# Kernel optimization log

Measured on AMD Instinct MI355X. Metric: run time of the kernel, lower is better.

## Reference

```python
import jax, jax.numpy as jnp
import numpy as np

BLOCK = 32       # MX block size
EMAX_E4M3 = 8.0  # max exponent of fp8 e4m3 (max normal = 448 = 1.75 * 2^8)
NUM_HEADS = 16


def _e4m3_round(v):
    """Round values to fp8 e4m3 grid (bias 7, 3 mantissa bits, subnormals, max 448)."""
    absv = jnp.abs(v)
    e = jnp.floor(jnp.log2(jnp.where(absv > 0, absv, 1.0)))
    e = jnp.maximum(e, -6.0)                # min normal exponent; below -> subnormal grid
    step = jnp.exp2(e - 3.0)                # 3 mantissa bits
    q = jnp.round(v / step) * step          # round-half-even like IEEE
    q = jnp.clip(q, -448.0, 448.0)
    return jnp.where(absv > 0, q, jnp.zeros_like(q))


def _mx_quantize(x):
    """Blockwise (32 along last dim) shared-exponent (E8M0) fp8 e4m3 quant-dequant."""
    shp = x.shape
    xb = x.reshape(shp[:-1] + (shp[-1] // BLOCK, BLOCK))
    amax = jnp.max(jnp.abs(xb), axis=-1, keepdims=True)
    sexp = jnp.floor(jnp.log2(jnp.where(amax > 0, amax, 1.0))) - EMAX_E4M3
    sexp = jnp.clip(sexp, -127.0, 127.0)    # E8M0 scale range
    scale = jnp.where(amax > 0, jnp.exp2(sexp), jnp.ones_like(sexp))
    q = _e4m3_round(xb / scale) * scale
    return q.reshape(shp)


def mxq(x):
    return _mx_quantize(x)


def _mx_linear(x, W, b):
    # quantize activations and weights (blocks of 32 along the contraction dim)
    return jnp.einsum('bse,oe->bso', mxq(x), mxq(W)) + b


def setup_inputs() -> dict:
    key = jax.random.key(0)
    ks = jax.random.split(key, 9)
    B, S, E = 4, 1024, 1024
    inp = {
        'query': jax.random.normal(ks[0], (B, S, E), dtype=jnp.float32),
        'Wq': jax.random.normal(ks[1], (E, E), dtype=jnp.float32) * 0.02,
        'bq': jnp.zeros((E,), dtype=jnp.float32),
        'Wk': jax.random.normal(ks[2], (E, E), dtype=jnp.float32) * 0.02,
        'bk': jnp.zeros((E,), dtype=jnp.float32),
        'Wv': jax.random.normal(ks[3], (E, E), dtype=jnp.float32) * 0.02,
        'bv': jnp.zeros((E,), dtype=jnp.float32),
        'Wo': jax.random.normal(ks[4], (E, E), dtype=jnp.float32) * 0.02,
        'bo': jnp.zeros((E,), dtype=jnp.float32),
    }
    return inp


def reference(query, Wq, bq, Wk, bk, Wv, bv, Wo, bo):
    B, S, E = query.shape
    H = NUM_HEADS
    D = E // H
    Q = _mx_linear(query, Wq, bq).reshape(B, S, H, D).transpose(0, 2, 1, 3)
    K = _mx_linear(query, Wk, bk).reshape(B, S, H, D).transpose(0, 2, 1, 3)
    V = _mx_linear(query, Wv, bv).reshape(B, S, H, D).transpose(0, 2, 1, 3)
    scores = jnp.einsum('bhqd,bhkd->bhqk', Q, K) / jnp.sqrt(jnp.float32(D))
    scores = mxq(scores)                    # score quantizer (blocks of 32 along kv dim)
    attn = jax.nn.softmax(scores, axis=-1)  # dropout p=0 -> identity
    ctx = jnp.einsum('bhqk,bhkd->bhqd', attn, V)
    ctx = ctx.transpose(0, 2, 1, 3).reshape(B, S, E)
    return _mx_linear(ctx, Wo, bo)
```

## Files before the change

kernel.cpp:

```cpp
#include <hip/hip_runtime.h>
#include <hip/hip_bf16.h>
#include <cstdint>
#include <cstddef>


#define S_LEN 1024
#define E_DIM 1024
#define NH    16
#define DH    64
#define BATCH 4
#define NROWS (BATCH * S_LEN)

typedef short          bf16x8  __attribute__((ext_vector_type(8)));
typedef float          f32x4   __attribute__((ext_vector_type(4)));
typedef unsigned short u16x8   __attribute__((ext_vector_type(8)));
typedef unsigned short u16x4   __attribute__((ext_vector_type(4)));
typedef unsigned int   u32x4   __attribute__((ext_vector_type(4)));


__device__ __forceinline__ void mx_scale_bits(float amax, float& scale, float& inv) {
  int eb = (int)(__float_as_uint(amax) >> 23);
  int sb = eb - 8;
  sb = sb < 1 ? 1 : (sb > 253 ? 253 : sb);
  float sc = __uint_as_float((unsigned)sb << 23);
  float iv = __uint_as_float((unsigned)(254 - sb) << 23);
  bool nz = (amax > 0.0f);
  scale = nz ? sc : 1.0f;
  inv   = nz ? iv : 1.0f;
}

__device__ __forceinline__ void qdq2(float& a, float& b) {
  a = fminf(fmaxf(a, -448.0f), 448.0f);
  b = fminf(fmaxf(b, -448.0f), 448.0f);
  int p = __builtin_amdgcn_cvt_pk_fp8_f32(a, b, 0, false);
  a = __builtin_amdgcn_cvt_f32_fp8(p, 0);
  b = __builtin_amdgcn_cvt_f32_fp8(p, 1);
}

__device__ __forceinline__ unsigned short f32_to_bf16_rne(float f) {
  unsigned u = __float_as_uint(f);
  unsigned r = 0x7FFFu + ((u >> 16) & 1u);
  return (unsigned short)((u + r) >> 16);
}

__device__ __forceinline__ float quad_red_max(float x) {
  auto p = __builtin_amdgcn_permlane16_swap(__float_as_uint(x), __float_as_uint(x), false, false);
  x = fmaxf(__uint_as_float(p[0]), __uint_as_float(p[1]));
  auto q = __builtin_amdgcn_permlane32_swap(__float_as_uint(x), __float_as_uint(x), false, false);
  return fmaxf(__uint_as_float(q[0]), __uint_as_float(q[1]));
}
__device__ __forceinline__ float quad_red_min(float x) {
  auto p = __builtin_amdgcn_permlane16_swap(__float_as_uint(x), __float_as_uint(x), false, false);
  x = fminf(__uint_as_float(p[0]), __uint_as_float(p[1]));
  auto q = __builtin_amdgcn_permlane32_swap(__float_as_uint(x), __float_as_uint(x), false, false);
  return fminf(__uint_as_float(q[0]), __uint_as_float(q[1]));
}
__device__ __forceinline__ float quad_red_sum(float x) {
  auto p = __builtin_amdgcn_permlane16_swap(__float_as_uint(x), __float_as_uint(x), false, false);
  x = __uint_as_float(p[0]) + __uint_as_float(p[1]);
  auto q = __builtin_amdgcn_permlane32_swap(__float_as_uint(x), __float_as_uint(x), false, false);
  return __uint_as_float(q[0]) + __uint_as_float(q[1]);
}


__device__ __forceinline__ void mxq_body(const float* __restrict__ in,
                                         unsigned short* __restrict__ out, int b) {
  const float4* p = (const float4*)(in + (size_t)b * 32);
  float v[32];
#pragma unroll
  for (int g = 0; g < 8; ++g) {
    float4 t = p[g];
    v[g * 4 + 0] = t.x; v[g * 4 + 1] = t.y; v[g * 4 + 2] = t.z; v[g * 4 + 3] = t.w;
  }
  float amax = 0.0f;
#pragma unroll
  for (int i = 0; i < 32; ++i) amax = fmaxf(amax, __builtin_fabsf(v[i]));
  float scale, inv;
  mx_scale_bits(amax, scale, inv);
  u16x8* q = (u16x8*)(out + (size_t)b * 32);
#pragma unroll
  for (int g = 0; g < 4; ++g) {
    u16x8 o;
#pragma unroll
    for (int e = 0; e < 8; e += 2) {
      float a = v[g * 8 + e] * inv, c = v[g * 8 + e + 1] * inv;
      qdq2(a, c);
      o[e]     = (unsigned short)(__float_as_uint(a * scale) >> 16);
      o[e + 1] = (unsigned short)(__float_as_uint(c * scale) >> 16);
    }
    q[g] = o;
  }
}

__global__ __launch_bounds__(256)
void mxq_all(const float* __restrict__ x,
             const float* __restrict__ w0, const float* __restrict__ w1,
             const float* __restrict__ w2, const float* __restrict__ w3,
             unsigned short* __restrict__ ox,
             unsigned short* __restrict__ o0, unsigned short* __restrict__ o1,
             unsigned short* __restrict__ o2, unsigned short* __restrict__ o3) {
  int blk = blockIdx.x;
  const float* in;
  unsigned short* out;
  int base;
  if (blk < 512)      { in = x;  out = ox; base = blk; }
  else if (blk < 640) { in = w0; out = o0; base = blk - 512; }
  else if (blk < 768) { in = w1; out = o1; base = blk - 640; }
  else if (blk < 896) { in = w2; out = o2; base = blk - 768; }
  else                { in = w3; out = o3; base = blk - 896; }
  mxq_body(in, out, base * 256 + threadIdx.x);
}


__global__ __launch_bounds__(256)
void gemm_qkv(const unsigned short* __restrict__ XQ,
              const unsigned short* __restrict__ Wqw, const unsigned short* __restrict__ Wkw,
              const unsigned short* __restrict__ Wvw,
              const float* __restrict__ bq, const float* __restrict__ bk,
              const float* __restrict__ bv,
              unsigned short* __restrict__ Qhi, unsigned short* __restrict__ Qlo,
              unsigned short* __restrict__ Khi, unsigned short* __restrict__ Klo,
              unsigned short* __restrict__ Vthi, unsigned short* __restrict__ Vtlo) {
  const int z = blockIdx.z;
  const unsigned short* Bw = (z == 0) ? Wqw : (z == 1) ? Wkw : Wvw;
  const float* bias = (z == 0) ? bq : (z == 1) ? bk : bv;
  unsigned short* Phi = (z == 0) ? Qhi : (z == 1) ? Khi : Vthi;
  unsigned short* Plo = (z == 0) ? Qlo : (z == 1) ? Klo : Vtlo;
  const float pre = (z == 0) ? 0.125f : 1.0f;

  __shared__ unsigned short sA[2][128 * 64];
  __shared__ unsigned short sB[2][128 * 64];
  const int tid = threadIdx.x;
  const int w = tid >> 6, ln = tid & 63;
  const int fid = blockIdx.y * 8 + blockIdx.x;
  const int xcd = fid & 7, sq = fid >> 3;
  const int bm = (xcd * 4 + (sq & 3)) * 128, bn = (sq >> 2) * 128;
  const int wm = (w >> 1) * 64, wn = (w & 1) * 64;
  const int quad = ln >> 4, col = ln & 15;

  f32x4 acc[4][4];
  f32x4 zero = {0.0f, 0.0f, 0.0f, 0.0f};
#pragma unroll
  for (int i = 0; i < 4; ++i)
#pragma unroll
    for (int j = 0; j < 4; ++j) acc[i][j] = zero;

  const int srow = ln >> 3;
  const int gsw  = (ln & 7) ^ srow;
  const int xo0 = (quad ^ (ln & 7)) * 8;
  const int xo1 = ((quad ^ 4) ^ (ln & 7)) * 8;

  auto STAGE = [&](int bb, int k0) {
#pragma unroll
    for (int q = 0; q < 4; ++q) {
      int row = w * 32 + q * 8 + srow;
      const unsigned short* ga = XQ + (size_t)(bm + row) * 1024 + k0 + gsw * 8;
      const unsigned short* gb = Bw + (size_t)(bn + row) * 1024 + k0 + gsw * 8;
      __builtin_amdgcn_global_load_lds(
          (const __attribute__((address_space(1))) unsigned int*)ga,
          (__attribute__((address_space(3))) unsigned int*)(&sA[bb][0] + (w * 32 + q * 8) * 64),
          16, 0, 0);
      __builtin_amdgcn_global_load_lds(
          (const __attribute__((address_space(1))) unsigned int*)gb,
          (__attribute__((address_space(3))) unsigned int*)(&sB[bb][0] + (w * 32 + q * 8) * 64),
          16, 0, 0);
    }
  };

  STAGE(0, 0);
#pragma unroll 1
  for (int k0 = 0; k0 < 1024; k0 += 64) {
    const int cur = (k0 >> 6) & 1;
    if (k0 < 960) {
      STAGE(cur ^ 1, k0 + 64);
      asm volatile("s_waitcnt vmcnt(8)" ::: "memory");
    } else {
      asm volatile("s_waitcnt vmcnt(0)" ::: "memory");
    }
    __builtin_amdgcn_s_barrier();
    __builtin_amdgcn_sched_barrier(0);

    const unsigned short* pA = &sA[cur][0];
    const unsigned short* pB = &sB[cur][0];
#pragma unroll
    for (int ks = 0; ks < 2; ++ks) {
      const int xo = ks ? xo1 : xo0;
      bf16x8 af[4], bfr[4];
#pragma unroll
      for (int t = 0; t < 4; ++t) {
        af[t]  = *(const bf16x8*)(pA + (wm + t * 16 + col) * 64 + xo);
        bfr[t] = *(const bf16x8*)(pB + (wn + t * 16 + col) * 64 + xo);
      }
#pragma unroll
      for (int ti = 0; ti < 4; ++ti)
#pragma unroll
        for (int tj = 0; tj < 4; ++tj)
          acc[ti][tj] = __builtin_amdgcn_mfma_f32_16x16x32_bf16(af[ti], bfr[tj], acc[ti][tj], 0, 0, 0);
    }
    __builtin_amdgcn_sched_barrier(0);
    __builtin_amdgcn_s_barrier();
  }

#pragma unroll
  for (int ti = 0; ti < 4; ++ti) {
#pragma unroll
    for (int tj = 0; tj < 4; ++tj) {
      int n = bn + wn + tj * 16 + col;
      float bv_ = bias[n];
      if (z != 2) {
#pragma unroll
        for (int i = 0; i < 4; ++i) {
          int m = bm + wm + ti * 16 + quad * 4 + i;
          float v = (acc[ti][tj][i] + bv_) * pre;
          unsigned short h = f32_to_bf16_rne(v);
          float hf = __uint_as_float((unsigned)h << 16);
          Phi[(size_t)m * 1024 + n] = h;
          Plo[(size_t)m * 1024 + n] = f32_to_bf16_rne(v - hf);
        }
      } else {
        int m0 = bm + wm + ti * 16 + quad * 4;
        u16x4 h4, l4;
#pragma unroll
        for (int i = 0; i < 4; ++i) {
          float v = acc[ti][tj][i] + bv_;
          unsigned short h = f32_to_bf16_rne(v);
          float hf = __uint_as_float((unsigned)h << 16);
          h4[i] = h;
          l4[i] = f32_to_bf16_rne(v - hf);
        }
        size_t idx = ((size_t)((m0 >> 10) * 1024 + n)) * 1024 + (m0 & 1023);
        *(u16x4*)(Phi + idx) = h4;
        *(u16x4*)(Plo + idx) = l4;
      }
    }
  }
}


__global__ __launch_bounds__(256)
void gemm_o(const unsigned short* __restrict__ A, const unsigned short* __restrict__ Bw,
            const float* __restrict__ bias, float* __restrict__ C) {
  __shared__ unsigned short sA[2][64 * 64];
  __shared__ unsigned short sB[2][128 * 64];
  const int tid = threadIdx.x;
  const int w = tid >> 6, ln = tid & 63;
  const int fid = blockIdx.y * 8 + blockIdx.x;
  const int xcd = fid & 7, sq = fid >> 3;
  const int bm = (xcd * 8 + (sq & 7)) * 64, bn = (sq >> 3) * 128;
  const int wr = (w >> 1) * 32, wc = (w & 1) * 64;
  const int quad = ln >> 4, col = ln & 15;

  f32x4 acc[2][4];
  f32x4 zero = {0.0f, 0.0f, 0.0f, 0.0f};
#pragma unroll
  for (int i = 0; i < 2; ++i)
#pragma unroll
    for (int j = 0; j < 4; ++j) acc[i][j] = zero;

  const int srow = ln >> 3;
  const int gsw  = (ln & 7) ^ srow;
  const int xo0 = (quad ^ (ln & 7)) * 8;
  const int xo1 = ((quad ^ 4) ^ (ln & 7)) * 8;

  auto STAGE = [&](int bb, int k0) {
#pragma unroll
    for (int qa = 0; qa < 2; ++qa) {
      int row = w * 16 + qa * 8 + srow;
      __builtin_amdgcn_global_load_lds(
          (const __attribute__((address_space(1))) unsigned int*)(A + (size_t)(bm + row) * 1024 + k0 + gsw * 8),
          (__attribute__((address_space(3))) unsigned int*)(&sA[bb][0] + (w * 16 + qa * 8) * 64),
          16, 0, 0);
    }
#pragma unroll
    for (int qb = 0; qb < 4; ++qb) {
      int row = w * 32 + qb * 8 + srow;
      __builtin_amdgcn_global_load_lds(
          (const __attribute__((address_space(1))) unsigned int*)(Bw + (size_t)(bn + row) * 1024 + k0 + gsw * 8),
          (__attribute__((address_space(3))) unsigned int*)(&sB[bb][0] + (w * 32 + qb * 8) * 64),
          16, 0, 0);
    }
  };

  STAGE(0, 0);
#pragma unroll 1
  for (int k0 = 0; k0 < 1024; k0 += 64) {
    const int cur = (k0 >> 6) & 1;
    if (k0 < 960) {
      STAGE(cur ^ 1, k0 + 64);
      asm volatile("s_waitcnt vmcnt(6)" ::: "memory");
    } else {
      asm volatile("s_waitcnt vmcnt(0)" ::: "memory");
    }
    __builtin_amdgcn_s_barrier();
    __builtin_amdgcn_sched_barrier(0);

    const unsigned short* pA = &sA[cur][0];
    const unsigned short* pB = &sB[cur][0];
#pragma unroll
    for (int ks = 0; ks < 2; ++ks) {
      const int xo = ks ? xo1 : xo0;
      bf16x8 af[2], bfr[4];
#pragma unroll
      for (int t = 0; t < 2; ++t)
        af[t] = *(const bf16x8*)(pA + (wr + t * 16 + col) * 64 + xo);
#pragma unroll
      for (int t = 0; t < 4; ++t)
        bfr[t] = *(const bf16x8*)(pB + (wc + t * 16 + col) * 64 + xo);
#pragma unroll
      for (int ti = 0; ti < 2; ++ti)
#pragma unroll
        for (int tj = 0; tj < 4; ++tj)
          acc[ti][tj] = __builtin_amdgcn_mfma_f32_16x16x32_bf16(af[ti], bfr[tj], acc[ti][tj], 0, 0, 0);
    }
    __builtin_amdgcn_sched_barrier(0);
    __builtin_amdgcn_s_barrier();
  }

#pragma unroll
  for (int ti = 0; ti < 2; ++ti) {
#pragma unroll
    for (int tj = 0; tj < 4; ++tj) {
      int n = bn + wc + tj * 16 + col;
      float bv_ = bias[n];
#pragma unroll
      for (int i = 0; i < 4; ++i) {
        int m = bm + wr + ti * 16 + quad * 4 + i;
        C[(size_t)m * 1024 + n] = acc[ti][tj][i] + bv_;
      }
    }
  }
}


__global__ __launch_bounds__(256, 4)
void attn_kernel(const unsigned short* __restrict__ Qhi, const unsigned short* __restrict__ Qlo,
                 const unsigned short* __restrict__ Khi, const unsigned short* __restrict__ Klo,
                 const unsigned short* __restrict__ Vthi, const unsigned short* __restrict__ Vtlo,
                 unsigned short* __restrict__ ctxq) {
  const int tid = threadIdx.x;
  const int id = blockIdx.y * 16 + blockIdx.x;
  const int qt = (id >> 3) & 15;
  const int bh = ((id >> 7) << 3) | (id & 7);
  const int b = bh >> 4, h = bh & 15;
  const int w = tid >> 6, ln = tid & 63, quad = ln >> 4, col = ln & 15;

  __shared__ __align__(16) short sK[16384];

  bf16x8 qh[2], ql[2];
  {
    const size_t qoff = (size_t)(b * 1024 + qt * 64 + w * 16 + col) * 1024 + h * 64 + quad * 8;
    qh[0] = *(const bf16x8*)(Qhi + qoff);
    qh[1] = *(const bf16x8*)(Qhi + qoff + 32);
    ql[0] = *(const bf16x8*)(Qlo + qoff);
    ql[1] = *(const bf16x8*)(Qlo + qoff + 32);
  }

  const unsigned short* gplane = (w == 0) ? Khi : (w == 1) ? Klo : (w == 2) ? Vthi : Vtlo;
  short* splane = sK + w * 4096;
  const int r8 = ln >> 3;
  const int ch = (ln & 7) ^ r8;
  const unsigned short* bp = (w < 2)
      ? gplane + (size_t)(b * 1024 + r8) * 1024 + h * 64 + ch * 8
      : gplane + (size_t)(b * 1024 + h * 64 + r8) * 1024 + ch * 8;
  const int ktstep = (w < 2) ? 65536 : 64;

  const int xo0 = (quad ^ (col & 7)) * 8;
  const int xo1 = ((quad + 4) ^ (col & 7)) * 8;

  f32x4 o[4];
  f32x4 zero = {0.0f, 0.0f, 0.0f, 0.0f};
#pragma unroll
  for (int t = 0; t < 4; ++t) o[t] = zero;
  float m_ = -3.0e38f, l_ = 0.0f;

  const float LOG2E = 1.44269504088896340736f;

#pragma unroll 1
  for (int kt = 0; kt < 16; ++kt) {
    __syncthreads();
#pragma unroll
    for (int g = 0; g < 8; ++g) {
      __builtin_amdgcn_global_load_lds(
          (const __attribute__((address_space(1))) unsigned int*)(bp + g * 8192),
          (__attribute__((address_space(3))) unsigned int*)(splane + g * 512),
          16, 0, 0);
    }
    bp += ktstep;
    __syncthreads();

    f32x4 s[4];
#pragma unroll
    for (int t = 0; t < 4; ++t) s[t] = zero;
#pragma unroll
    for (int t = 0; t < 4; ++t) {
      const int rb = (t * 16 + col) * 64;
#pragma unroll
      for (int ks = 0; ks < 2; ++ks) {
        const int xo = ks ? xo1 : xo0;
        bf16x8 kh = *(const bf16x8*)(sK +        rb + xo);
        bf16x8 kl = *(const bf16x8*)(sK + 4096 + rb + xo);
        s[t] = __builtin_amdgcn_mfma_f32_16x16x32_bf16(kh, ql[ks], s[t], 0, 0, 0);
        s[t] = __builtin_amdgcn_mfma_f32_16x16x32_bf16(kl, qh[ks], s[t], 0, 0, 0);
        s[t] = __builtin_amdgcn_mfma_f32_16x16x32_bf16(kh, qh[ks], s[t], 0, 0, 0);
      }
    }

    float mx0 = fmaxf(fmaxf(fmaxf(s[0][0], s[0][1]), fmaxf(s[0][2], s[0][3])),
                      fmaxf(fmaxf(s[1][0], s[1][1]), fmaxf(s[1][2], s[1][3])));
    float mn0 = fminf(fminf(fminf(s[0][0], s[0][1]), fminf(s[0][2], s[0][3])),
                      fminf(fminf(s[1][0], s[1][1]), fminf(s[1][2], s[1][3])));
    float mx1 = fmaxf(fmaxf(fmaxf(s[2][0], s[2][1]), fmaxf(s[2][2], s[2][3])),
                      fmaxf(fmaxf(s[3][0], s[3][1]), fmaxf(s[3][2], s[3][3])));
    float mn1 = fminf(fminf(fminf(s[2][0], s[2][1]), fminf(s[2][2], s[2][3])),
                      fminf(fminf(s[3][0], s[3][1]), fminf(s[3][2], s[3][3])));
    mx0 = quad_red_max(mx0); mn0 = quad_red_min(mn0);
    mx1 = quad_red_max(mx1); mn1 = quad_red_min(mn1);

    float sc0, iv0, sc1, iv1;
    mx_scale_bits(fmaxf(mx0, -mn0), sc0, iv0);
    mx_scale_bits(fmaxf(mx1, -mn1), sc1, iv1);
    float scl0 = sc0 * LOG2E, scl1 = sc1 * LOG2E;
#pragma unroll
    for (int t = 0; t < 4; ++t) {
      float iv  = (t < 2) ? iv0 : iv1;
      float scl = (t < 2) ? scl0 : scl1;
      float q0 = s[t][0] * iv, q1 = s[t][1] * iv;
      qdq2(q0, q1);
      float q2 = s[t][2] * iv, q3 = s[t][3] * iv;
      qdq2(q2, q3);
      s[t][0] = q0 * scl; s[t][1] = q1 * scl;
      s[t][2] = q2 * scl; s[t][3] = q3 * scl;
    }
    float d0 = mx0 * iv0, d1 = mx1 * iv1;
    qdq2(d0, d1);
    float mt = fmaxf(d0 * scl0, d1 * scl1);

    if (__any(mt > m_ + 4.0f)) {
      float mnew  = fmaxf(m_, mt);
      float alpha = __builtin_amdgcn_exp2f(m_ - mnew);
      m_ = mnew;
      l_ *= alpha;
#pragma unroll
      for (int nt = 0; nt < 4; ++nt)
#pragma unroll
        for (int i = 0; i < 4; ++i) o[nt][i] *= alpha;
    }
#pragma unroll
    for (int t = 0; t < 4; ++t) {
      float p0 = __builtin_amdgcn_exp2f(s[t][0] - m_);
      float p1 = __builtin_amdgcn_exp2f(s[t][1] - m_);
      float p2 = __builtin_amdgcn_exp2f(s[t][2] - m_);
      float p3 = __builtin_amdgcn_exp2f(s[t][3] - m_);
      s[t][0] = p0; s[t][1] = p1; s[t][2] = p2; s[t][3] = p3;
      l_ += (p0 + p1) + (p2 + p3);
    }

    unsigned Wh[4][2], Wl[4][2];
#pragma unroll
    for (int t = 0; t < 4; ++t) {
#pragma unroll
      for (int u = 0; u < 2; ++u) {
        float a = s[t][2 * u], c = s[t][2 * u + 1];
        __hip_bfloat162 h2 = __float22bfloat162_rn(make_float2(a, c));
        unsigned uh = *(unsigned*)&h2;
        float af = __uint_as_float(uh << 16);
        float cf = __uint_as_float(uh & 0xffff0000u);
        __hip_bfloat162 l2 = __float22bfloat162_rn(make_float2(a - af, c - cf));
        Wh[t][u] = uh;
        Wl[t][u] = *(unsigned*)&l2;
      }
    }
    bf16x8 pah[2], pal[2];
#pragma unroll
    for (int ks = 0; ks < 2; ++ks) {
      auto a0  = __builtin_amdgcn_permlane32_swap(Wh[2 * ks][0], Wh[2 * ks + 1][0], false, false);
      auto j02 = __builtin_amdgcn_permlane16_swap(a0[0], a0[1], false, false);
      auto a1  = __builtin_amdgcn_permlane32_swap(Wh[2 * ks][1], Wh[2 * ks + 1][1], false, false);
      auto j13 = __builtin_amdgcn_permlane16_swap(a1[0], a1[1], false, false);
      u32x4 hw; hw[0] = j02[0]; hw[1] = j13[0]; hw[2] = j02[1]; hw[3] = j13[1];
      pah[ks] = __builtin_bit_cast(bf16x8, hw);
      auto b0  = __builtin_amdgcn_permlane32_swap(Wl[2 * ks][0], Wl[2 * ks + 1][0], false, false);
      auto k02 = __builtin_amdgcn_permlane16_swap(b0[0], b0[1], false, false);
      auto b1  = __builtin_amdgcn_permlane32_swap(Wl[2 * ks][1], Wl[2 * ks + 1][1], false, false);
      auto k13 = __builtin_amdgcn_permlane16_swap(b1[0], b1[1], false, false);
      u32x4 lw; lw[0] = k02[0]; lw[1] = k13[0]; lw[2] = k02[1]; lw[3] = k13[1];
      pal[ks] = __builtin_bit_cast(bf16x8, lw);
    }

#pragma unroll
    for (int nt = 0; nt < 4; ++nt) {
      const int rb = (nt * 16 + col) * 64;
#pragma unroll
      for (int ks = 0; ks < 2; ++ks) {
        const int xo = ks ? xo1 : xo0;
        bf16x8 vh = *(const bf16x8*)(sK +  8192 + rb + xo);
        bf16x8 vl = *(const bf16x8*)(sK + 12288 + rb + xo);
        o[nt] = __builtin_amdgcn_mfma_f32_16x16x32_bf16(vh, pal[ks], o[nt], 0, 0, 0);
        o[nt] = __builtin_amdgcn_mfma_f32_16x16x32_bf16(vl, pah[ks], o[nt], 0, 0, 0);
        o[nt] = __builtin_amdgcn_mfma_f32_16x16x32_bf16(vh, pah[ks], o[nt], 0, 0, 0);
      }
    }
  }

  float linv = 1.0f / quad_red_sum(l_);
#pragma unroll
  for (int nt = 0; nt < 4; ++nt)
#pragma unroll
    for (int i = 0; i < 4; ++i) o[nt][i] *= linv;

  float am0 = 0.0f, am1 = 0.0f;
#pragma unroll
  for (int i = 0; i < 4; ++i) {
    am0 = fmaxf(am0, fmaxf(__builtin_fabsf(o[0][i]), __builtin_fabsf(o[1][i])));
    am1 = fmaxf(am1, fmaxf(__builtin_fabsf(o[2][i]), __builtin_fabsf(o[3][i])));
  }
  am0 = quad_red_max(am0);
  am1 = quad_red_max(am1);
  float sc0, iv0, sc1, iv1;
  mx_scale_bits(am0, sc0, iv0);
  mx_scale_bits(am1, sc1, iv1);

  const int tok = b * 1024 + qt * 64 + w * 16 + col;
  const size_t base = (size_t)tok * 1024 + h * 64 + quad * 4;
#pragma unroll
  for (int nt = 0; nt < 4; ++nt) {
    float iv = (nt < 2) ? iv0 : iv1;
    float sc = (nt < 2) ? sc0 : sc1;
    float q0 = o[nt][0] * iv, q1 = o[nt][1] * iv;
    qdq2(q0, q1);
    float q2 = o[nt][2] * iv, q3 = o[nt][3] * iv;
    qdq2(q2, q3);
    u16x4 h4;
    h4[0] = (unsigned short)(__float_as_uint(q0 * sc) >> 16);
    h4[1] = (unsigned short)(__float_as_uint(q1 * sc) >> 16);
    h4[2] = (unsigned short)(__float_as_uint(q2 * sc) >> 16);
    h4[3] = (unsigned short)(__float_as_uint(q3 * sc) >> 16);
    *(u16x4*)(ctxq + base + nt * 16) = h4;
  }
}


extern "C" void kernel_launch(void* const* d_in, const int* in_sizes, int n_in,
                              void* d_out, int out_size, void* d_ws, size_t ws_size,
                              hipStream_t stream) {
  (void)in_sizes; (void)n_in; (void)out_size; (void)ws_size;
  const float* x  = (const float*)d_in[0];
  const float* Wq = (const float*)d_in[1];
  const float* bq = (const float*)d_in[2];
  const float* Wk = (const float*)d_in[3];
  const float* bk = (const float*)d_in[4];
  const float* Wv = (const float*)d_in[5];
  const float* bv = (const float*)d_in[6];
  const float* Wo = (const float*)d_in[7];
  const float* bo = (const float*)d_in[8];

  char* wsb = (char*)d_ws;
  const size_t MB = (size_t)1 << 20;
  unsigned short* XQb   = (unsigned short*)(wsb + 0);
  unsigned short* WQb   = (unsigned short*)(wsb + 8 * MB);
  unsigned short* WKb   = (unsigned short*)(wsb + 10 * MB);
  unsigned short* WVb   = (unsigned short*)(wsb + 12 * MB);
  unsigned short* WOb   = (unsigned short*)(wsb + 14 * MB);
  unsigned short* Qhi   = (unsigned short*)(wsb + 16 * MB);
  unsigned short* Qlo   = (unsigned short*)(wsb + 24 * MB);
  unsigned short* Khi   = (unsigned short*)(wsb + 32 * MB);
  unsigned short* Klo   = (unsigned short*)(wsb + 40 * MB);
  unsigned short* Vthi  = (unsigned short*)(wsb + 48 * MB);
  unsigned short* Vtlo  = (unsigned short*)(wsb + 56 * MB);
  unsigned short* CTXQb = XQb;

  mxq_all<<<1024, 256, 0, stream>>>(x, Wq, Wk, Wv, Wo, XQb, WQb, WKb, WVb, WOb);

  dim3 qkvgrid(E_DIM / 128, NROWS / 128, 3);
  gemm_qkv<<<qkvgrid, 256, 0, stream>>>(XQb, WQb, WKb, WVb, bq, bk, bv,
                                        Qhi, Qlo, Khi, Klo, Vthi, Vtlo);

  dim3 agrid(16, 64);
  attn_kernel<<<agrid, 256, 0, stream>>>(Qhi, Qlo, Khi, Klo, Vthi, Vtlo, CTXQb);

  dim3 ogrid(E_DIM / 128, NROWS / 64);
  gemm_o<<<ogrid, 256, 0, stream>>>(CTXQb, WOb, bo, (float*)d_out);
}
```

Baseline: 222.2 us.

## Triple-buffer QKV GEMM with BK=32 and overlap K/V loads in attention

```diff
diff --git a/kernel.cpp b/kernel.cpp
--- a/kernel.cpp
+++ b/kernel.cpp
@@ -128,8 +128,8 @@
   unsigned short* Plo = (z == 0) ? Qlo : (z == 1) ? Klo : Vtlo;
   const float pre = (z == 0) ? 0.125f : 1.0f;
 
-  __shared__ unsigned short sA[2][128 * 64];
-  __shared__ unsigned short sB[2][128 * 64];
+  __shared__ unsigned short sA[3][128 * 32];
+  __shared__ unsigned short sB[3][128 * 32];
   const int tid = threadIdx.x;
   const int w = tid >> 6, ln = tid & 63;
   const int fid = blockIdx.y * 8 + blockIdx.x;
@@ -145,60 +145,62 @@
 #pragma unroll
     for (int j = 0; j < 4; ++j) acc[i][j] = zero;
 
-  const int srow = ln >> 3;
-  const int gsw  = (ln & 7) ^ srow;
-  const int xo0 = (quad ^ (ln & 7)) * 8;
-  const int xo1 = ((quad ^ 4) ^ (ln & 7)) * 8;
+  const int rl = ln >> 2;
+  const int cc = (ln & 3) ^ ((ln >> 3) & 3);
+  const int xoq = ((quad ^ (col >> 1)) & 3) * 8;
 
   auto STAGE = [&](int bb, int k0) {
 #pragma unroll
-    for (int q = 0; q < 4; ++q) {
-      int row = w * 32 + q * 8 + srow;
-      const unsigned short* ga = XQ + (size_t)(bm + row) * 1024 + k0 + gsw * 8;
-      const unsigned short* gb = Bw + (size_t)(bn + row) * 1024 + k0 + gsw * 8;
+    for (int j = 0; j < 2; ++j) {
+      int row = (w * 2 + j) * 16 + rl;
       __builtin_amdgcn_global_load_lds(
-          (const __attribute__((address_space(1))) unsigned int*)ga,
-          (__attribute__((address_space(3))) unsigned int*)(&sA[bb][0] + (w * 32 + q * 8) * 64),
+          (const __attribute__((address_space(1))) unsigned int*)(XQ + (size_t)(bm + row) * 1024 + k0 + cc * 8),
+          (__attribute__((address_space(3))) unsigned int*)(&sA[bb][0] + (w * 2 + j) * 512 + ln * 8),
           16, 0, 0);
+    }
+#pragma unroll
+    for (int j = 0; j < 2; ++j) {
+      int row = (w * 2 + j) * 16 + rl;
       __builtin_amdgcn_global_load_lds(
-          (const __attribute__((address_space(1))) unsigned int*)gb,
-          (__attribute__((address_space(3))) unsigned int*)(&sB[bb][0] + (w * 32 + q * 8) * 64),
+          (const __attribute__((address_space(1))) unsigned int*)(Bw + (size_t)(bn + row) * 1024 + k0 + cc * 8),
+          (__attribute__((address_space(3))) unsigned int*)(&sB[bb][0] + (w * 2 + j) * 512 + ln * 8),
           16, 0, 0);
     }
   };
 
   STAGE(0, 0);
+  STAGE(1, 32);
+  int b0 = 0, b1 = 1, b2 = 2;
 #pragma unroll 1
-  for (int k0 = 0; k0 < 1024; k0 += 64) {
-    const int cur = (k0 >> 6) & 1;
-    if (k0 < 960) {
-      STAGE(cur ^ 1, k0 + 64);
+  for (int it = 0; it < 32; ++it) {
+    if (it < 30) {
+      STAGE(b2, (it + 2) * 32);
       asm volatile("s_waitcnt vmcnt(8)" ::: "memory");
+    } else if (it == 30) {
+      asm volatile("s_waitcnt vmcnt(4)" ::: "memory");
     } else {
       asm volatile("s_waitcnt vmcnt(0)" ::: "memory");
     }
     __builtin_amdgcn_s_barrier();
     __builtin_amdgcn_sched_barrier(0);
 
-    const unsigned short* pA = &sA[cur][0];
-    const unsigned short* pB = &sB[cur][0];
-#pragma unroll
-    for (int ks = 0; ks < 2; ++ks) {
-      const int xo = ks ? xo1 : xo0;
-      bf16x8 af[4], bfr[4];
-#pragma unroll
-      for (int t = 0; t < 4; ++t) {
-        af[t]  = *(const bf16x8*)(pA + (wm + t * 16 + col) * 64 + xo);
-        bfr[t] = *(const bf16x8*)(pB + (wn + t * 16 + col) * 64 + xo);
-      }
-#pragma unroll
-      for (int ti = 0; ti < 4; ++ti)
-#pragma unroll
-        for (int tj = 0; tj < 4; ++tj)
-          acc[ti][tj] = __builtin_amdgcn_mfma_f32_16x16x32_bf16(af[ti], bfr[tj], acc[ti][tj], 0, 0, 0);
-    }
-    __builtin_amdgcn_sched_barrier(0);
-    __builtin_amdgcn_s_barrier();
+    const unsigned short* pA = &sA[b0][0];
+    const unsigned short* pB = &sB[b0][0];
+    bf16x8 af[4], bfr[4];
+#pragma unroll
+    for (int t = 0; t < 4; ++t) {
+      af[t]  = *(const bf16x8*)(pA + (wm + t * 16 + col) * 32 + xoq);
+      bfr[t] = *(const bf16x8*)(pB + (wn + t * 16 + col) * 32 + xoq);
+    }
+#pragma unroll
+    for (int ti = 0; ti < 4; ++ti)
+#pragma unroll
+      for (int tj = 0; tj < 4; ++tj)
+        acc[ti][tj] = __builtin_amdgcn_mfma_f32_16x16x32_bf16(af[ti], bfr[tj], acc[ti][tj], 0, 0, 0);
+
+    __builtin_amdgcn_sched_barrier(0);
+    __builtin_amdgcn_s_barrier();
+    int tmp = b0; b0 = b1; b1 = b2; b2 = tmp;
   }
 
 #pragma unroll
@@ -375,9 +377,7 @@
 
   const float LOG2E = 1.44269504088896340736f;
 
-#pragma unroll 1
-  for (int kt = 0; kt < 16; ++kt) {
-    __syncthreads();
+  auto STAGE = [&]() {
 #pragma unroll
     for (int g = 0; g < 8; ++g) {
       __builtin_amdgcn_global_load_lds(
@@ -385,8 +385,17 @@
           (__attribute__((address_space(3))) unsigned int*)(splane + g * 512),
           16, 0, 0);
     }
-    bp += ktstep;
-    __syncthreads();
+  };
+
+  asm volatile("s_waitcnt vmcnt(0)" ::: "memory");
+  STAGE();
+  bp += ktstep;
+
+#pragma unroll 1
+  for (int kt = 0; kt < 16; ++kt) {
+    if (w < 2) asm volatile("s_waitcnt vmcnt(0)" ::: "memory");
+    __builtin_amdgcn_s_barrier();
+    __builtin_amdgcn_sched_barrier(0);
 
     f32x4 s[4];
 #pragma unroll
@@ -404,6 +413,9 @@
         s[t] = __builtin_amdgcn_mfma_f32_16x16x32_bf16(kh, qh[ks], s[t], 0, 0, 0);
       }
     }
+    __builtin_amdgcn_sched_barrier(0);
+    __builtin_amdgcn_s_barrier();
+    if (kt < 15 && w < 2) STAGE();
 
     float mx0 = fmaxf(fmaxf(fmaxf(s[0][0], s[0][1]), fmaxf(s[0][2], s[0][3])),
                       fmaxf(fmaxf(s[1][0], s[1][1]), fmaxf(s[1][2], s[1][3])));
@@ -422,14 +434,12 @@
     float scl0 = sc0 * LOG2E, scl1 = sc1 * LOG2E;
 #pragma unroll
     for (int t = 0; t < 4; ++t) {
-      float iv  = (t < 2) ? iv0 : iv1;
-      float scl = (t < 2) ? scl0 : scl1;
+      float iv = (t < 2) ? iv0 : iv1;
       float q0 = s[t][0] * iv, q1 = s[t][1] * iv;
       qdq2(q0, q1);
       float q2 = s[t][2] * iv, q3 = s[t][3] * iv;
       qdq2(q2, q3);
-      s[t][0] = q0 * scl; s[t][1] = q1 * scl;
-      s[t][2] = q2 * scl; s[t][3] = q3 * scl;
+      s[t][0] = q0; s[t][1] = q1; s[t][2] = q2; s[t][3] = q3;
     }
     float d0 = mx0 * iv0, d1 = mx1 * iv1;
     qdq2(d0, d1);
@@ -447,10 +457,11 @@
     }
 #pragma unroll
     for (int t = 0; t < 4; ++t) {
-      float p0 = __builtin_amdgcn_exp2f(s[t][0] - m_);
-      float p1 = __builtin_amdgcn_exp2f(s[t][1] - m_);
-      float p2 = __builtin_amdgcn_exp2f(s[t][2] - m_);
-      float p3 = __builtin_amdgcn_exp2f(s[t][3] - m_);
+      float scl = (t < 2) ? scl0 : scl1;
+      float p0 = __builtin_amdgcn_exp2f(__builtin_fmaf(s[t][0], scl, -m_));
+      float p1 = __builtin_amdgcn_exp2f(__builtin_fmaf(s[t][1], scl, -m_));
+      float p2 = __builtin_amdgcn_exp2f(__builtin_fmaf(s[t][2], scl, -m_));
+      float p3 = __builtin_amdgcn_exp2f(__builtin_fmaf(s[t][3], scl, -m_));
       s[t][0] = p0; s[t][1] = p1; s[t][2] = p2; s[t][3] = p3;
       l_ += (p0 + p1) + (p2 + p3);
     }
@@ -487,6 +498,10 @@
       pal[ks] = __builtin_bit_cast(bf16x8, lw);
     }
 
+    if (w >= 2) asm volatile("s_waitcnt vmcnt(0)" ::: "memory");
+    __builtin_amdgcn_s_barrier();
+    __builtin_amdgcn_sched_barrier(0);
+
 #pragma unroll
     for (int nt = 0; nt < 4; ++nt) {
       const int rb = (nt * 16 + col) * 64;
@@ -500,6 +515,10 @@
         o[nt] = __builtin_amdgcn_mfma_f32_16x16x32_bf16(vh, pah[ks], o[nt], 0, 0, 0);
       }
     }
+    __builtin_amdgcn_sched_barrier(0);
+    __builtin_amdgcn_s_barrier();
+    if (kt < 15 && w >= 2) STAGE();
+    bp += ktstep;
   }
 
   float linv = 1.0f / quad_red_sum(l_);
```

After: 235.7 us. 6.1% more time.

## Process two query subtiles per attention block to reuse staged K/V tiles

Applied to the files above, without the earlier changes.

```diff
diff --git a/kernel.cpp b/kernel.cpp
--- a/kernel.cpp
+++ b/kernel.cpp
@@ -244,9 +244,7 @@
   __shared__ unsigned short sB[2][128 * 64];
   const int tid = threadIdx.x;
   const int w = tid >> 6, ln = tid & 63;
-  const int fid = blockIdx.y * 8 + blockIdx.x;
-  const int xcd = fid & 7, sq = fid >> 3;
-  const int bm = (xcd * 8 + (sq & 7)) * 64, bn = (sq >> 3) * 128;
+  const int bm = blockIdx.y * 64, bn = blockIdx.x * 128;
   const int wr = (w >> 1) * 32, wc = (w & 1) * 64;
   const int quad = ln >> 4, col = ln & 15;
 
@@ -332,27 +330,29 @@
 }
 
 
-__global__ __launch_bounds__(256, 4)
+__global__ __launch_bounds__(256, 2)
 void attn_kernel(const unsigned short* __restrict__ Qhi, const unsigned short* __restrict__ Qlo,
                  const unsigned short* __restrict__ Khi, const unsigned short* __restrict__ Klo,
                  const unsigned short* __restrict__ Vthi, const unsigned short* __restrict__ Vtlo,
                  unsigned short* __restrict__ ctxq) {
   const int tid = threadIdx.x;
   const int id = blockIdx.y * 16 + blockIdx.x;
-  const int qt = (id >> 3) & 15;
-  const int bh = ((id >> 7) << 3) | (id & 7);
+  const int qt = (id >> 3) & 7;
+  const int bh = ((id >> 6) << 3) | (id & 7);
   const int b = bh >> 4, h = bh & 15;
   const int w = tid >> 6, ln = tid & 63, quad = ln >> 4, col = ln & 15;
 
   __shared__ __align__(16) short sK[16384];
 
-  bf16x8 qh[2], ql[2];
-  {
-    const size_t qoff = (size_t)(b * 1024 + qt * 64 + w * 16 + col) * 1024 + h * 64 + quad * 8;
-    qh[0] = *(const bf16x8*)(Qhi + qoff);
-    qh[1] = *(const bf16x8*)(Qhi + qoff + 32);
-    ql[0] = *(const bf16x8*)(Qlo + qoff);
-    ql[1] = *(const bf16x8*)(Qlo + qoff + 32);
+  bf16x8 qh[2][2], ql[2][2];
+#pragma unroll
+  for (int sub = 0; sub < 2; ++sub) {
+    const size_t qoff =
+        (size_t)(b * 1024 + qt * 128 + sub * 64 + w * 16 + col) * 1024 + h * 64 + quad * 8;
+    qh[sub][0] = *(const bf16x8*)(Qhi + qoff);
+    qh[sub][1] = *(const bf16x8*)(Qhi + qoff + 32);
+    ql[sub][0] = *(const bf16x8*)(Qlo + qoff);
+    ql[sub][1] = *(const bf16x8*)(Qlo + qoff + 32);
   }
 
   const unsigned short* gplane = (w == 0) ? Khi : (w == 1) ? Klo : (w == 2) ? Vthi : Vtlo;
@@ -367,11 +367,13 @@
   const int xo0 = (quad ^ (col & 7)) * 8;
   const int xo1 = ((quad + 4) ^ (col & 7)) * 8;
 
-  f32x4 o[4];
+  f32x4 o[2][4];
   f32x4 zero = {0.0f, 0.0f, 0.0f, 0.0f};
 #pragma unroll
-  for (int t = 0; t < 4; ++t) o[t] = zero;
-  float m_ = -3.0e38f, l_ = 0.0f;
+  for (int sub = 0; sub < 2; ++sub)
+#pragma unroll
+    for (int t = 0; t < 4; ++t) o[sub][t] = zero;
+  float m_[2] = {-3.0e38f, -3.0e38f}, l_[2] = {0.0f, 0.0f};
 
   const float LOG2E = 1.44269504088896340736f;
 
@@ -388,9 +390,11 @@
     bp += ktstep;
     __syncthreads();
 
-    f32x4 s[4];
-#pragma unroll
-    for (int t = 0; t < 4; ++t) s[t] = zero;
+    f32x4 s[2][4];
+#pragma unroll
+    for (int sub = 0; sub < 2; ++sub)
+#pragma unroll
+      for (int t = 0; t < 4; ++t) s[sub][t] = zero;
 #pragma unroll
     for (int t = 0; t < 4; ++t) {
       const int rb = (t * 16 + col) * 64;
@@ -399,92 +403,97 @@
         const int xo = ks ? xo1 : xo0;
         bf16x8 kh = *(const bf16x8*)(sK +        rb + xo);
         bf16x8 kl = *(const bf16x8*)(sK + 4096 + rb + xo);
-        s[t] = __builtin_amdgcn_mfma_f32_16x16x32_bf16(kh, ql[ks], s[t], 0, 0, 0);
-        s[t] = __builtin_amdgcn_mfma_f32_16x16x32_bf16(kl, qh[ks], s[t], 0, 0, 0);
-        s[t] = __builtin_amdgcn_mfma_f32_16x16x32_bf16(kh, qh[ks], s[t], 0, 0, 0);
-      }
-    }
-
-    float mx0 = fmaxf(fmaxf(fmaxf(s[0][0], s[0][1]), fmaxf(s[0][2], s[0][3])),
-                      fmaxf(fmaxf(s[1][0], s[1][1]), fmaxf(s[1][2], s[1][3])));
-    float mn0 = fminf(fminf(fminf(s[0][0], s[0][1]), fminf(s[0][2], s[0][3])),
-                      fminf(fminf(s[1][0], s[1][1]), fminf(s[1][2], s[1][3])));
-    float mx1 = fmaxf(fmaxf(fmaxf(s[2][0], s[2][1]), fmaxf(s[2][2], s[2][3])),
-                      fmaxf(fmaxf(s[3][0], s[3][1]), fmaxf(s[3][2], s[3][3])));
-    float mn1 = fminf(fminf(fminf(s[2][0], s[2][1]), fminf(s[2][2], s[2][3])),
-                      fminf(fminf(s[3][0], s[3][1]), fminf(s[3][2], s[3][3])));
-    mx0 = quad_red_max(mx0); mn0 = quad_red_min(mn0);
-    mx1 = quad_red_max(mx1); mn1 = quad_red_min(mn1);
-
-    float sc0, iv0, sc1, iv1;
-    mx_scale_bits(fmaxf(mx0, -mn0), sc0, iv0);
-    mx_scale_bits(fmaxf(mx1, -mn1), sc1, iv1);
-    float scl0 = sc0 * LOG2E, scl1 = sc1 * LOG2E;
-#pragma unroll
-    for (int t = 0; t < 4; ++t) {
-      float iv  = (t < 2) ? iv0 : iv1;
-      float scl = (t < 2) ? scl0 : scl1;
-      float q0 = s[t][0] * iv, q1 = s[t][1] * iv;
-      qdq2(q0, q1);
-      float q2 = s[t][2] * iv, q3 = s[t][3] * iv;
-      qdq2(q2, q3);
-      s[t][0] = q0 * scl; s[t][1] = q1 * scl;
-      s[t][2] = q2 * scl; s[t][3] = q3 * scl;
-    }
-    float d0 = mx0 * iv0, d1 = mx1 * iv1;
-    qdq2(d0, d1);
-    float mt = fmaxf(d0 * scl0, d1 * scl1);
-
-    if (__any(mt > m_ + 4.0f)) {
-      float mnew  = fmaxf(m_, mt);
-      float alpha = __builtin_amdgcn_exp2f(m_ - mnew);
-      m_ = mnew;
-      l_ *= alpha;
-#pragma unroll
-      for (int nt = 0; nt < 4; ++nt)
-#pragma unroll
-        for (int i = 0; i < 4; ++i) o[nt][i] *= alpha;
-    }
-#pragma unroll
-    for (int t = 0; t < 4; ++t) {
-      float p0 = __builtin_amdgcn_exp2f(s[t][0] - m_);
-      float p1 = __builtin_amdgcn_exp2f(s[t][1] - m_);
-      float p2 = __builtin_amdgcn_exp2f(s[t][2] - m_);
-      float p3 = __builtin_amdgcn_exp2f(s[t][3] - m_);
-      s[t][0] = p0; s[t][1] = p1; s[t][2] = p2; s[t][3] = p3;
-      l_ += (p0 + p1) + (p2 + p3);
-    }
-
-    unsigned Wh[4][2], Wl[4][2];
-#pragma unroll
-    for (int t = 0; t < 4; ++t) {
-#pragma unroll
-      for (int u = 0; u < 2; ++u) {
-        float a = s[t][2 * u], c = s[t][2 * u + 1];
-        __hip_bfloat162 h2 = __float22bfloat162_rn(make_float2(a, c));
-        unsigned uh = *(unsigned*)&h2;
-        float af = __uint_as_float(uh << 16);
-        float cf = __uint_as_float(uh & 0xffff0000u);
-        __hip_bfloat162 l2 = __float22bfloat162_rn(make_float2(a - af, c - cf));
-        Wh[t][u] = uh;
-        Wl[t][u] = *(unsigned*)&l2;
-      }
-    }
-    bf16x8 pah[2], pal[2];
-#pragma unroll
-    for (int ks = 0; ks < 2; ++ks) {
-      auto a0  = __builtin_amdgcn_permlane32_swap(Wh[2 * ks][0], Wh[2 * ks + 1][0], false, false);
-      auto j02 = __builtin_amdgcn_permlane16_swap(a0[0], a0[1], false, false);
-      auto a1  = __builtin_amdgcn_permlane32_swap(Wh[2 * ks][1], Wh[2 * ks + 1][1], false, false);
-      auto j13 = __builtin_amdgcn_permlane16_swap(a1[0], a1[1], false, false);
-      u32x4 hw; hw[0] = j02[0]; hw[1] = j13[0]; hw[2] = j02[1]; hw[3] = j13[1];
-      pah[ks] = __builtin_bit_cast(bf16x8, hw);
-      auto b0  = __builtin_amdgcn_permlane32_swap(Wl[2 * ks][0], Wl[2 * ks + 1][0], false, false);
-      auto k02 = __builtin_amdgcn_permlane16_swap(b0[0], b0[1], false, false);
-      auto b1  = __builtin_amdgcn_permlane32_swap(Wl[2 * ks][1], Wl[2 * ks + 1][1], false, false);
-      auto k13 = __builtin_amdgcn_permlane16_swap(b1[0], b1[1], false, false);
-      u32x4 lw; lw[0] = k02[0]; lw[1] = k13[0]; lw[2] = k02[1]; lw[3] = k13[1];
-      pal[ks] = __builtin_bit_cast(bf16x8, lw);
+#pragma unroll
+        for (int sub = 0; sub < 2; ++sub) {
+          s[sub][t] = __builtin_amdgcn_mfma_f32_16x16x32_bf16(kh, ql[sub][ks], s[sub][t], 0, 0, 0);
+          s[sub][t] = __builtin_amdgcn_mfma_f32_16x16x32_bf16(kl, qh[sub][ks], s[sub][t], 0, 0, 0);
+          s[sub][t] = __builtin_amdgcn_mfma_f32_16x16x32_bf16(kh, qh[sub][ks], s[sub][t], 0, 0, 0);
+        }
+      }
+    }
+
+    bf16x8 pah[2][2], pal[2][2];
+#pragma unroll
+    for (int sub = 0; sub < 2; ++sub) {
+      float mx0 = fmaxf(fmaxf(fmaxf(s[sub][0][0], s[sub][0][1]), fmaxf(s[sub][0][2], s[sub][0][3])),
+                        fmaxf(fmaxf(s[sub][1][0], s[sub][1][1]), fmaxf(s[sub][1][2], s[sub][1][3])));
+      float mn0 = fminf(fminf(fminf(s[sub][0][0], s[sub][0][1]), fminf(s[sub][0][2], s[sub][0][3])),
+                        fminf(fminf(s[sub][1][0], s[sub][1][1]), fminf(s[sub][1][2], s[sub][1][3])));
+      float mx1 = fmaxf(fmaxf(fmaxf(s[sub][2][0], s[sub][2][1]), fmaxf(s[sub][2][2], s[sub][2][3])),
+                        fmaxf(fmaxf(s[sub][3][0], s[sub][3][1]), fmaxf(s[sub][3][2], s[sub][3][3])));
+      float mn1 = fminf(fminf(fminf(s[sub][2][0], s[sub][2][1]), fminf(s[sub][2][2], s[sub][2][3])),
+                        fminf(fminf(s[sub][3][0], s[sub][3][1]), fminf(s[sub][3][2], s[sub][3][3])));
+      mx0 = quad_red_max(mx0); mn0 = quad_red_min(mn0);
+      mx1 = quad_red_max(mx1); mn1 = quad_red_min(mn1);
+
+      float sc0, iv0, sc1, iv1;
+      mx_scale_bits(fmaxf(mx0, -mn0), sc0, iv0);
+      mx_scale_bits(fmaxf(mx1, -mn1), sc1, iv1);
+      float scl0 = sc0 * LOG2E, scl1 = sc1 * LOG2E;
+#pragma unroll
+      for (int t = 0; t < 4; ++t) {
+        float iv = (t < 2) ? iv0 : iv1;
+        float q0 = s[sub][t][0] * iv, q1 = s[sub][t][1] * iv;
+        qdq2(q0, q1);
+        float q2 = s[sub][t][2] * iv, q3 = s[sub][t][3] * iv;
+        qdq2(q2, q3);
+        s[sub][t][0] = q0; s[sub][t][1] = q1; s[sub][t][2] = q2; s[sub][t][3] = q3;
+      }
+      float d0 = mx0 * iv0, d1 = mx1 * iv1;
+      qdq2(d0, d1);
+      float mt = fmaxf(d0 * scl0, d1 * scl1);
+
+      if (__any(mt > m_[sub] + 4.0f)) {
+        float mnew  = fmaxf(m_[sub], mt);
+        float alpha = __builtin_amdgcn_exp2f(m_[sub] - mnew);
+        m_[sub] = mnew;
+        l_[sub] *= alpha;
+#pragma unroll
+        for (int nt = 0; nt < 4; ++nt)
+#pragma unroll
+          for (int i = 0; i < 4; ++i) o[sub][nt][i] *= alpha;
+      }
+#pragma unroll
+      for (int t = 0; t < 4; ++t) {
+        float scl = (t < 2) ? scl0 : scl1;
+        float p0 = __builtin_amdgcn_exp2f(__builtin_fmaf(s[sub][t][0], scl, -m_[sub]));
+        float p1 = __builtin_amdgcn_exp2f(__builtin_fmaf(s[sub][t][1], scl, -m_[sub]));
+        float p2 = __builtin_amdgcn_exp2f(__builtin_fmaf(s[sub][t][2], scl, -m_[sub]));
+        float p3 = __builtin_amdgcn_exp2f(__builtin_fmaf(s[sub][t][3], scl, -m_[sub]));
+        s[sub][t][0] = p0; s[sub][t][1] = p1; s[sub][t][2] = p2; s[sub][t][3] = p3;
+        l_[sub] += (p0 + p1) + (p2 + p3);
+      }
+
+      unsigned Wh[4][2], Wl[4][2];
+#pragma unroll
+      for (int t = 0; t < 4; ++t) {
+#pragma unroll
+        for (int u = 0; u < 2; ++u) {
+          float a = s[sub][t][2 * u], c = s[sub][t][2 * u + 1];
+          __hip_bfloat162 h2 = __float22bfloat162_rn(make_float2(a, c));
+          unsigned uh = *(unsigned*)&h2;
+          float af = __uint_as_float(uh << 16);
+          float cf = __uint_as_float(uh & 0xffff0000u);
+          __hip_bfloat162 l2 = __float22bfloat162_rn(make_float2(a - af, c - cf));
+          Wh[t][u] = uh;
+          Wl[t][u] = *(unsigned*)&l2;
+        }
+      }
+#pragma unroll
+      for (int ks = 0; ks < 2; ++ks) {
+        auto a0  = __builtin_amdgcn_permlane32_swap(Wh[2 * ks][0], Wh[2 * ks + 1][0], false, false);
+        auto j02 = __builtin_amdgcn_permlane16_swap(a0[0], a0[1], false, false);
+        auto a1  = __builtin_amdgcn_permlane32_swap(Wh[2 * ks][1], Wh[2 * ks + 1][1], false, false);
+        auto j13 = __builtin_amdgcn_permlane16_swap(a1[0], a1[1], false, false);
+        u32x4 hw; hw[0] = j02[0]; hw[1] = j13[0]; hw[2] = j02[1]; hw[3] = j13[1];
+        pah[sub][ks] = __builtin_bit_cast(bf16x8, hw);
+        auto b0  = __builtin_amdgcn_permlane32_swap(Wl[2 * ks][0], Wl[2 * ks + 1][0], false, false);
+        auto k02 = __builtin_amdgcn_permlane16_swap(b0[0], b0[1], false, false);
+        auto b1  = __builtin_amdgcn_permlane32_swap(Wl[2 * ks][1], Wl[2 * ks + 1][1], false, false);
+        auto k13 = __builtin_amdgcn_permlane16_swap(b1[0], b1[1], false, false);
+        u32x4 lw; lw[0] = k02[0]; lw[1] = k13[0]; lw[2] = k02[1]; lw[3] = k13[1];
+        pal[sub][ks] = __builtin_bit_cast(bf16x8, lw);
+      }
     }
 
 #pragma unroll
@@ -495,47 +504,53 @@
         const int xo = ks ? xo1 : xo0;
         bf16x8 vh = *(const bf16x8*)(sK +  8192 + rb + xo);
         bf16x8 vl = *(const bf16x8*)(sK + 12288 + rb + xo);
-        o[nt] = __builtin_amdgcn_mfma_f32_16x16x32_bf16(vh, pal[ks], o[nt], 0, 0, 0);
-        o[nt] = __builtin_amdgcn_mfma_f32_16x16x32_bf16(vl, pah[ks], o[nt], 0, 0, 0);
-        o[nt] = __builtin_amdgcn_mfma_f32_16x16x32_bf16(vh, pah[ks], o[nt], 0, 0, 0);
-      }
-    }
-  }
-
-  float linv = 1.0f / quad_red_sum(l_);
-#pragma unroll
-  for (int nt = 0; nt < 4; ++nt)
-#pragma unroll
-    for (int i = 0; i < 4; ++i) o[nt][i] *= linv;
-
-  float am0 = 0.0f, am1 = 0.0f;
-#pragma unroll
-  for (int i = 0; i < 4; ++i) {
-    am0 = fmaxf(am0, fmaxf(__builtin_fabsf(o[0][i]), __builtin_fabsf(o[1][i])));
-    am1 = fmaxf(am1, fmaxf(__builtin_fabsf(o[2][i]), __builtin_fabsf(o[3][i])));
-  }
-  am0 = quad_red_max(am0);
-  am1 = quad_red_max(am1);
-  float sc0, iv0, sc1, iv1;
-  mx_scale_bits(am0, sc0, iv0);
-  mx_scale_bits(am1, sc1, iv1);
-
-  const int tok = b * 1024 + qt * 64 + w * 16 + col;
-  const size_t base = (size_t)tok * 1024 + h * 64 + quad * 4;
-#pragma unroll
-  for (int nt = 0; nt < 4; ++nt) {
-    float iv = (nt < 2) ? iv0 : iv1;
-    float sc = (nt < 2) ? sc0 : sc1;
-    float q0 = o[nt][0] * iv, q1 = o[nt][1] * iv;
-    qdq2(q0, q1);
-    float q2 = o[nt][2] * iv, q3 = o[nt][3] * iv;
-    qdq2(q2, q3);
-    u16x4 h4;
-    h4[0] = (unsigned short)(__float_as_uint(q0 * sc) >> 16);
-    h4[1] = (unsigned short)(__float_as_uint(q1 * sc) >> 16);
-    h4[2] = (unsigned short)(__float_as_uint(q2 * sc) >> 16);
-    h4[3] = (unsigned short)(__float_as_uint(q3 * sc) >> 16);
-    *(u16x4*)(ctxq + base + nt * 16) = h4;
+#pragma unroll
+        for (int sub = 0; sub < 2; ++sub) {
+          o[sub][nt] = __builtin_amdgcn_mfma_f32_16x16x32_bf16(vh, pal[sub][ks], o[sub][nt], 0, 0, 0);
+          o[sub][nt] = __builtin_amdgcn_mfma_f32_16x16x32_bf16(vl, pah[sub][ks], o[sub][nt], 0, 0, 0);
+          o[sub][nt] = __builtin_amdgcn_mfma_f32_16x16x32_bf16(vh, pah[sub][ks], o[sub][nt], 0, 0, 0);
+        }
+      }
+    }
+  }
+
+#pragma unroll
+  for (int sub = 0; sub < 2; ++sub) {
+    float linv = 1.0f / quad_red_sum(l_[sub]);
+#pragma unroll
+    for (int nt = 0; nt < 4; ++nt)
+#pragma unroll
+      for (int i = 0; i < 4; ++i) o[sub][nt][i] *= linv;
+
+    float am0 = 0.0f, am1 = 0.0f;
+#pragma unroll
+    for (int i = 0; i < 4; ++i) {
+      am0 = fmaxf(am0, fmaxf(__builtin_fabsf(o[sub][0][i]), __builtin_fabsf(o[sub][1][i])));
+      am1 = fmaxf(am1, fmaxf(__builtin_fabsf(o[sub][2][i]), __builtin_fabsf(o[sub][3][i])));
+    }
+    am0 = quad_red_max(am0);
+    am1 = quad_red_max(am1);
+    float sc0, iv0, sc1, iv1;
+    mx_scale_bits(am0, sc0, iv0);
+    mx_scale_bits(am1, sc1, iv1);
+
+    const int tok = b * 1024 + qt * 128 + sub * 64 + w * 16 + col;
+    const size_t base = (size_t)tok * 1024 + h * 64 + quad * 4;
+#pragma unroll
+    for (int nt = 0; nt < 4; ++nt) {
+      float iv = (nt < 2) ? iv0 : iv1;
+      float sc = (nt < 2) ? sc0 : sc1;
+      float q0 = o[sub][nt][0] * iv, q1 = o[sub][nt][1] * iv;
+      qdq2(q0, q1);
+      float q2 = o[sub][nt][2] * iv, q3 = o[sub][nt][3] * iv;
+      qdq2(q2, q3);
+      u16x4 h4;
+      h4[0] = (unsigned short)(__float_as_uint(q0 * sc) >> 16);
+      h4[1] = (unsigned short)(__float_as_uint(q1 * sc) >> 16);
+      h4[2] = (unsigned short)(__float_as_uint(q2 * sc) >> 16);
+      h4[3] = (unsigned short)(__float_as_uint(q3 * sc) >> 16);
+      *(u16x4*)(ctxq + base + nt * 16) = h4;
+    }
   }
 }
 
@@ -575,7 +590,7 @@
   gemm_qkv<<<qkvgrid, 256, 0, stream>>>(XQb, WQb, WKb, WVb, bq, bk, bv,
                                         Qhi, Qlo, Khi, Klo, Vthi, Vtlo);
 
-  dim3 agrid(16, 64);
+  dim3 agrid(16, 32);
   attn_kernel<<<agrid, 256, 0, stream>>>(Qhi, Qlo, Khi, Klo, Vthi, Vtlo, CTXQb);
 
   dim3 ogrid(E_DIM / 128, NROWS / 64);
```

Measured after the change: 229.9 us. 1.03x slower.
